# Kernel optimization log

Measured on AMD Instinct MI355X. Metric: run time of the kernel, lower is better.

The kernel has to match this reference:

```python
import jax, jax.numpy as jnp
import numpy as np

B, NWORD, HID = 4, 24, 512


def setup_inputs() -> dict:
    key = jax.random.key(0)
    ks = jax.random.split(key, 7)
    H = HID
    scale_in = 1.0 / np.sqrt(H)
    return {
        "seqt": jax.random.normal(ks[0], (B, NWORD, 2 * H), dtype=jnp.float32),
        # ins_input_linearity: Linear(H -> 5H) with bias
        "Wi": jax.random.normal(ks[1], (5 * H, H), dtype=jnp.float32) * scale_in,
        "bi": jnp.zeros((5 * H,), dtype=jnp.float32),
        # ins_state_linearity: Linear(H -> 5H) with bias (bias init: forget slots = 1)
        "Ws": jax.random.normal(ks[2], (5 * H, H), dtype=jnp.float32) * scale_in,
        "bs": jnp.zeros((5 * H,), dtype=jnp.float32).at[H:2 * H].set(1.0),
        # ins_bilinearity: BilinearSimilarity(2H, 2H) -> scalar x^T W y
        "Wbil": jax.random.normal(ks[3], (2 * H, 2 * H), dtype=jnp.float32) * (1.0 / (2.0 * H)),
    }


def reference(seqt, Wi, bi, Ws, bs, Wbil):
    """Inside pass (do_inside) of DioLstm in training mode (soft_sum over splits).

    Chart cell (left, L) covers words [left, left+L]. Returns root v = concat(h, c).
    """
    Bn, n, twoH = seqt.shape
    H = twoH // 2
    # ins_bias buffer: ones on the two forget-gate slots [H:3H]
    ins_bias = jnp.zeros((5 * H,), dtype=seqt.dtype).at[H:3 * H].set(1.0)

    def single(seq):  # seq: [n, 2H]
        chartH = jnp.zeros((n, n, H), seq.dtype).at[:, 0].set(seq[:, :H])
        chartC = jnp.zeros((n, n, H), seq.dtype).at[:, 0].set(seq[:, H:])
        chartS = jnp.zeros((n, n), seq.dtype)  # leaf scores are 0
        for L in range(1, n):  # span length - 1 (static unroll over diagonals)
            P = n - L  # number of spans on this diagonal
            lefts = jnp.arange(P)[:, None]          # [P,1]
            ksplit = jnp.arange(L)[None, :]          # [1,L]
            # left child: (left, k); right child: (left+k+1, L-1-k)
            lH = chartH[lefts, ksplit]; lC = chartC[lefts, ksplit]; lS = chartS[lefts, ksplit]
            ridx = lefts + ksplit + 1
            rlen = jnp.broadcast_to(L - 1 - ksplit, ridx.shape)
            rH = chartH[ridx, rlen]; rC = chartC[ridx, rlen]; rS = chartS[ridx, rlen]
            lv = jnp.concatenate([lH, lC], axis=-1)  # [P,L,2H]
            rv = jnp.concatenate([rH, rC], axis=-1)
            # bilinear compatibility + child scores
            compat = jnp.einsum('pki,ij,pkj->pk', lv, Wbil, rv) + lS + rS  # [P,L]
            # projected_input + projected_state (sum once; gate slices of the sum)
            proj = (lH @ Wi.T + bi + ins_bias) + (rH @ Ws.T + bs)  # [P,L,5H]
            ig, lf, rf, g, og = jnp.split(proj, 5, axis=-1)
            ig = jax.nn.sigmoid(ig); lf = jax.nn.sigmoid(lf); rf = jax.nn.sigmoid(rf)
            g = jnp.tanh(g); og = jax.nn.sigmoid(og)
            mem = lf * lC + rf * rC + ig * g
            h = og * jnp.tanh(mem)  # [P,L,H]
            # soft_sum: torch.tensor(s_set) detaches scores -> stop_gradient on weights
            sw = jax.lax.stop_gradient(compat)
            w = jax.nn.softmax(sw, axis=-1)  # [P,L]
            Hnew = jnp.einsum('pk,pkh->ph', w, h)
            Cnew = jnp.einsum('pk,pkh->ph', w, mem)
            Snew = jnp.sum(w * sw, axis=-1)
            pidx = jnp.arange(P)
            chartH = chartH.at[pidx, L].set(Hnew)
            chartC = chartC.at[pidx, L].set(Cnew)
            chartS = chartS.at[pidx, L].set(Snew)
        # root cell v = concat(h, c)
        return jnp.concatenate([chartH[0, n - 1], chartC[0, n - 1]], axis=0)

    return jax.vmap(single)(seqt)  # [B, 2H]
```

## Files before the change

kernel.cpp:

```cpp
#include <hip/hip_runtime.h>
#include <math.h>

#define NB 4
#define NW 24
#define H 512
#define H2 1024
#define H5 2560
#define NCELL 300
#define NEED_BYTES ((size_t)72<<20)

static float* g_buf = nullptr;
__attribute__((constructor)) static void dio_alloc_ws(){
  (void)hipMalloc((void**)&g_buf, NEED_BYTES);
}

typedef __attribute__((ext_vector_type(8))) short bf16x8;
typedef __attribute__((ext_vector_type(4))) float f32x4;
typedef unsigned short ushort_t;

__device__ __forceinline__ int coff(int l){ return l*NW - (l*(l-1))/2; }
__device__ __forceinline__ float sigm(float x){ return 1.f/(1.f+__expf(-x)); }
__device__ __forceinline__ float ftanh(float x){ return 1.f - 2.f/(__expf(2.f*x)+1.f); }

__device__ __forceinline__ ushort_t f2b(float x){
  unsigned int u = __float_as_uint(x);
  u += 0x7FFF + ((u>>16)&1);
  return (ushort_t)(u>>16);
}
__device__ __forceinline__ float b2f(ushort_t h){
  return __uint_as_float(((unsigned int)h)<<16);
}
__device__ __forceinline__ void split_store(ushort_t* __restrict__ ph,
                                            ushort_t* __restrict__ pl,
                                            size_t idx, float x){
  ushort_t h = f2b(x);
  ph[idx] = h;
  pl[idx] = f2b(x - b2f(h));
}

__device__ __forceinline__ float compat_dot(const float* __restrict__ cU,
                                            const float* __restrict__ cH,
                                            const float* __restrict__ cC,
                                            const float* __restrict__ cS,
                                            int lc, int rc, int lane){
  const float4* U4  = (const float4*)(cU + (size_t)lc*H2);
  const float4* Hr4 = (const float4*)(cH + (size_t)rc*H);
  const float4* Cr4 = (const float4*)(cC + (size_t)rc*H);
  float p = 0.f;
  #pragma unroll
  for (int it=0; it<2; it++){
    float4 u = U4[lane + 64*it], h = Hr4[lane + 64*it];
    p += u.x*h.x + u.y*h.y + u.z*h.z + u.w*h.w;
  }
  #pragma unroll
  for (int it=0; it<2; it++){
    float4 u = U4[128 + lane + 64*it], c = Cr4[lane + 64*it];
    p += u.x*c.x + u.y*c.y + u.z*c.z + u.w*c.w;
  }
  #pragma unroll
  for (int off=32; off>0; off>>=1) p += __shfl_down(p, off);
  return p + cS[lc] + cS[rc];
}

__global__ void k_init(const float* __restrict__ seqt,
                       const float* __restrict__ Wi, const float* __restrict__ Ws,
                       const float* __restrict__ Wbil,
                       ushort_t* __restrict__ WiBh, ushort_t* __restrict__ WiBl,
                       ushort_t* __restrict__ WsBh, ushort_t* __restrict__ WsBl,
                       ushort_t* __restrict__ WbilTh, ushort_t* __restrict__ WbilTl,
                       float* __restrict__ cH, float* __restrict__ cC, float* __restrict__ cS,
                       ushort_t* __restrict__ cHbh, ushort_t* __restrict__ cHbl,
                       ushort_t* __restrict__ cCbh, ushort_t* __restrict__ cCbl){
  const int blk = blockIdx.x, t = threadIdx.x;
  if (blk < 10240){
    int i = blk*256 + t;
    const int n = H5*H;
    if (i < n) split_store(WiBh, WiBl, i, Wi[i]);
    else       split_store(WsBh, WsBl, i-n, Ws[i-n]);
  } else if (blk < 11264){
    __shared__ float tile[32][33];
    int tb = blk - 10240;
    int tr = (tb>>5)*32, tc = (tb&31)*32;
    int tx = t & 31, ty = t >> 5;
    #pragma unroll
    for (int i=0;i<32;i+=8)
      tile[ty+i][tx] = Wbil[(size_t)(tr+ty+i)*H2 + tc+tx];
    __syncthreads();
    #pragma unroll
    for (int i=0;i<32;i+=8)
      split_store(WbilTh, WbilTl, (size_t)(tc+ty+i)*H2 + tr+tx, tile[tx][ty+i]);
  } else {
    int tid = (blk-11264)*256 + t;
    if (tid < NB*NW*H){
      int b = tid/(NW*H); int r = tid%(NW*H); int i = r/H; int d = r%H;
      size_t idx = (size_t)(b*NCELL + i)*H + d;
      float hv = seqt[(size_t)(b*NW+i)*H2 + d];
      float cv = seqt[(size_t)(b*NW+i)*H2 + H + d];
      cH[idx]=hv; cC[idx]=cv;
      split_store(cHbh,cHbl,idx,hv);
      split_store(cCbh,cCbl,idx,cv);
      if (d==0) cS[b*NCELL+i] = 0.f;
    }
  }
}

__device__ __forceinline__ void mfma3(f32x4& acc, bf16x8 ah, bf16x8 al,
                                      bf16x8 bh, bf16x8 bl){
  acc = __builtin_amdgcn_mfma_f32_16x16x32_bf16(ah, bh, acc, 0,0,0);
  acc = __builtin_amdgcn_mfma_f32_16x16x32_bf16(ah, bl, acc, 0,0,0);
  acc = __builtin_amdgcn_mfma_f32_16x16x32_bf16(al, bh, acc, 0,0,0);
}

__global__ void __launch_bounds__(512)
k_projN(const ushort_t* __restrict__ WiBh, const ushort_t* __restrict__ WiBl,
        const ushort_t* __restrict__ WsBh, const ushort_t* __restrict__ WsBl,
        const ushort_t* __restrict__ WbilTh, const ushort_t* __restrict__ WbilTl,
        const float* __restrict__ bi, const float* __restrict__ bs,
        const ushort_t* __restrict__ cHbh, const ushort_t* __restrict__ cHbl,
        const ushort_t* __restrict__ cCbh, const ushort_t* __restrict__ cCbl,
        float* __restrict__ cPI, float* __restrict__ cPS, float* __restrict__ cU,
        int d, int P)
{
  __shared__ f32x4 red[8][64];
  const int t = threadIdx.x, wave = t>>6, lane = t&63;
  const int jt = blockIdx.x;
  const int m0 = blockIdx.y*16;
  const int Mtot = NB*P;
  const int nm = min(16, Mtot-m0);

  int kind, j0;
  if (jt < 160){ kind=0; j0 = jt*16; }
  else if (jt < 320){ kind=1; j0 = (jt-160)*16; }
  else { kind=2; j0 = (jt-320)*16; }

  const int r = lane & 15;
  const int q = lane >> 4;

  int mg = m0 + (r < nm ? r : 0);
  const size_t arow = (size_t)((mg/P)*NCELL + coff(d) + mg%P)*H;

  f32x4 acc = {0.f,0.f,0.f,0.f};

  if (kind < 2){
    const ushort_t* bh_ = (kind==0 ? WiBh : WsBh) + (size_t)(j0+r)*H;
    const ushort_t* bl_ = (kind==0 ? WiBl : WsBl) + (size_t)(j0+r)*H;
    const int ks = wave*64 + q*8;
    bf16x8 fah[2], fal[2], fbh[2], fbl[2];
    #pragma unroll
    for (int s=0;s<2;s++){
      const int ko = ks + s*32;
      fah[s] = *(const bf16x8*)(cHbh + arow + ko);
      fal[s] = *(const bf16x8*)(cHbl + arow + ko);
      fbh[s] = *(const bf16x8*)(bh_ + ko);
      fbl[s] = *(const bf16x8*)(bl_ + ko);
    }
    #pragma unroll
    for (int s=0;s<2;s++) mfma3(acc, fah[s], fal[s], fbh[s], fbl[s]);
  } else {
    const ushort_t* bh_ = WbilTh + (size_t)(j0+r)*H2;
    const ushort_t* bl_ = WbilTl + (size_t)(j0+r)*H2;
    const ushort_t* ah_ = (wave<4 ? cHbh : cCbh) + arow;
    const ushort_t* al_ = (wave<4 ? cHbl : cCbl) + arow;
    const int kg0 = wave*128;
    const int ka0 = kg0 & 511;
    bf16x8 fah[4], fal[4], fbh[4], fbl[4];
    #pragma unroll
    for (int s=0;s<4;s++){
      const int so = s*32 + q*8;
      fah[s] = *(const bf16x8*)(ah_ + ka0 + so);
      fal[s] = *(const bf16x8*)(al_ + ka0 + so);
      fbh[s] = *(const bf16x8*)(bh_ + kg0 + so);
      fbl[s] = *(const bf16x8*)(bl_ + kg0 + so);
    }
    #pragma unroll
    for (int s=0;s<4;s++) mfma3(acc, fah[s], fal[s], fbh[s], fbl[s]);
  }

  red[wave][lane] = acc;
  __syncthreads();
  if (wave == 0){
    f32x4 s0=red[0][lane], s1=red[1][lane], s2=red[2][lane], s3=red[3][lane];
    f32x4 s4=red[4][lane], s5=red[5][lane], s6=red[6][lane], s7=red[7][lane];
    f32x4 tot = ((s0+s1)+(s2+s3)) + ((s4+s5)+(s6+s7));
    const int jo = j0 + r;
    float bias = 0.f;
    if (kind==0) bias = bi[jo] + ((jo>=H && jo<3*H)?1.f:0.f);
    else if (kind==1) bias = bs[jo];
    #pragma unroll
    for (int reg=0; reg<4; reg++){
      const int m = q*4 + reg;
      if (m < nm){
        const int mg2 = m0 + m;
        const size_t cell = (size_t)((mg2/P)*NCELL + coff(d) + mg2%P);
        const float v = tot[reg];
        if (kind==0)      cPI[cell*H5 + jo] = v + bias;
        else if (kind==1) cPS[cell*H5 + jo] = v + bias;
        else              cU [cell*H2 + jo] = v;
      }
    }
  }
}

__global__ void __launch_bounds__(256)
k_combine3(const float* __restrict__ cPI, const float* __restrict__ cPS,
           const float* __restrict__ cU,
           float* __restrict__ cH, float* __restrict__ cC, float* __restrict__ cS,
           ushort_t* __restrict__ cHbh, ushort_t* __restrict__ cHbl,
           ushort_t* __restrict__ cCbh, ushort_t* __restrict__ cCbl,
           const float* __restrict__ compatR, float* __restrict__ compatW,
           int L, int P){
  const int t = threadIdx.x;
  const int lane = t & 63;
  const int wave = t >> 6;
  const int nphase = NB*P*16;
  const int blk = blockIdx.x;

  if (blk >= nphase){
    const int P1 = P-1;
    const int nterm = L-1;
    int tid = (blk-nphase)*4 + wave;
    if (P1 > 0 && nterm > 0 && tid < NB*P1*nterm){
      int cell1 = tid / nterm;
      int k = 1 + tid % nterm;
      int b = cell1 / P1, left = cell1 % P1;
      int lc = b*NCELL + coff(k) + left;
      int rc = b*NCELL + coff(L-k) + left+k+1;
      float v = compat_dot(cU, cH, cC, cS, lc, rc, lane);
      if (lane==0) compatW[(b*NW + left)*NW + k] = v;
    }
    return;
  }

  const int cellid = blk >> 4;
  const int dg = blk & 15;
  const int b = cellid / P;
  const int left = cellid % P;
  __shared__ float compat_s[32];
  __shared__ float wts_s[32];
  __shared__ float S_s;
  __shared__ float partH[8][32];
  __shared__ float partC[8][32];

  if (wave == 0){
    int lc = b*NCELL + left;
    int rc = b*NCELL + coff(L-1) + left+1;
    float v = compat_dot(cU, cH, cC, cS, lc, rc, lane);
    if (lane==0) compat_s[0] = v;
  } else if (wave == 1 && L >= 2){
    int lc = b*NCELL + coff(L-1) + left;
    int rc = b*NCELL + left+L;
    float v = compat_dot(cU, cH, cC, cS, lc, rc, lane);
    if (lane==0) compat_s[L-1] = v;
  }
  if (t >= 1 && t <= L-2) compat_s[t] = compatR[(b*NW + left)*NW + t];
  __syncthreads();
  if (t==0){
    float mx = -1e30f;
    for (int k=0;k<L;k++) mx = fmaxf(mx, compat_s[k]);
    float den = 0.f;
    for (int k=0;k<L;k++){ float e = __expf(compat_s[k]-mx); wts_s[k]=e; den+=e; }
    float inv = 1.f/den, S = 0.f;
    for (int k=0;k<L;k++){ wts_s[k]*=inv; S += wts_s[k]*compat_s[k]; }
    S_s = S;
  }
  __syncthreads();
  const int dloc = t & 31;
  const int dim = dg*32 + dloc;
  const int kpar = t >> 5;
  float aH = 0.f, aC = 0.f;
  for (int k=kpar; k<L; k+=8){
    float wk = wts_s[k];
    int lc = b*NCELL + coff(k) + left;
    int rc = b*NCELL + coff(L-1-k) + left+k+1;
    const float* PI = cPI + (size_t)lc*H5;
    const float* PS = cPS + (size_t)rc*H5;
    float p0 = PI[dim]     + PS[dim];
    float p1 = PI[H+dim]   + PS[H+dim];
    float p2 = PI[2*H+dim] + PS[2*H+dim];
    float p3 = PI[3*H+dim] + PS[3*H+dim];
    float p4 = PI[4*H+dim] + PS[4*H+dim];
    float lcv = cC[(size_t)lc*H + dim];
    float rcv = cC[(size_t)rc*H + dim];
    float mem = sigm(p1)*lcv + sigm(p2)*rcv + sigm(p0)*ftanh(p3);
    float h = sigm(p4)*ftanh(mem);
    aH += wk*h; aC += wk*mem;
  }
  if (kpar > 0){ partH[kpar][dloc]=aH; partC[kpar][dloc]=aC; }
  __syncthreads();
  if (kpar == 0){
    #pragma unroll
    for (int q=1;q<8;q++){ aH += partH[q][dloc]; aC += partC[q][dloc]; }
    size_t nc = (size_t)(b*NCELL + coff(L) + left);
    cH[nc*H + dim] = aH;
    cC[nc*H + dim] = aC;
    split_store(cHbh,cHbl, nc*H + dim, aH);
    split_store(cCbh,cCbl, nc*H + dim, aC);
    if (t==0 && dg==0) cS[nc] = S_s;
  }
}

__global__ void k_out(const float* __restrict__ cH, const float* __restrict__ cC,
                      float* __restrict__ out){
  int tid = blockIdx.x*256+threadIdx.x;
  if (tid >= NB*H2) return;
  int b = tid>>10, d = tid&1023;
  int cell = b*NCELL + 299;
  out[tid] = (d<H) ? cH[(size_t)cell*H + d] : cC[(size_t)cell*H + (d-H)];
}

extern "C" void kernel_launch(void* const* d_in, const int* in_sizes, int n_in,
                              void* d_out, int out_size, void* d_ws, size_t ws_size,
                              hipStream_t stream){
  const float* seqt = (const float*)d_in[0];
  const float* Wi   = (const float*)d_in[1];
  const float* bi   = (const float*)d_in[2];
  const float* Ws   = (const float*)d_in[3];
  const float* bs   = (const float*)d_in[4];
  const float* Wbil = (const float*)d_in[5];
  float* out = (float*)d_out;

  float* p = (ws_size >= NEED_BYTES && g_buf == nullptr) ? (float*)d_ws : g_buf;
  float* cH  = p; p += (size_t)NB*NCELL*H;
  float* cC  = p; p += (size_t)NB*NCELL*H;
  float* cS  = p; p += (size_t)NB*NCELL;
  float* cPI = p; p += (size_t)NB*NCELL*H5;
  float* cPS = p; p += (size_t)NB*NCELL*H5;
  float* cU  = p; p += (size_t)NB*NCELL*H2;
  float* compatA = p; p += (size_t)NB*NW*NW;
  float* compatB = p; p += (size_t)NB*NW*NW;
  ushort_t* u = (ushort_t*)p;
  ushort_t* WiBh   = u; u += (size_t)H5*H;
  ushort_t* WiBl   = u; u += (size_t)H5*H;
  ushort_t* WsBh   = u; u += (size_t)H5*H;
  ushort_t* WsBl   = u; u += (size_t)H5*H;
  ushort_t* WbilTh = u; u += (size_t)H2*H2;
  ushort_t* WbilTl = u; u += (size_t)H2*H2;
  ushort_t* cHbh   = u; u += (size_t)NB*NCELL*H;
  ushort_t* cHbl   = u; u += (size_t)NB*NCELL*H;
  ushort_t* cCbh   = u; u += (size_t)NB*NCELL*H;
  ushort_t* cCbl   = u; u += (size_t)NB*NCELL*H;

  k_init<<<11456, 256, 0, stream>>>(seqt, Wi, Ws, Wbil,
      WiBh, WiBl, WsBh, WsBl, WbilTh, WbilTl,
      cH, cC, cS, cHbh, cHbl, cCbh, cCbl);

  k_projN<<<dim3(384, (NB*NW+15)/16), 512, 0, stream>>>(
      WiBh, WiBl, WsBh, WsBl, WbilTh, WbilTl, bi, bs,
      cHbh, cHbl, cCbh, cCbl, cPI, cPS, cU, 0, NW);
  for (int L=1; L<NW; L++){
    int P = NW - L;
    int P1 = P-1, nterm = L-1;
    int wblk = (P1>0 && nterm>0) ? (NB*P1*nterm + 3)/4 : 0;
    float* bufR = (L&1) ? compatA : compatB;
    float* bufW = (L&1) ? compatB : compatA;
    k_combine3<<<NB*P*16 + wblk, 256, 0, stream>>>(
        cPI, cPS, cU, cH, cC, cS, cHbh, cHbl, cCbh, cCbl,
        bufR, bufW, L, P);
    if (L < NW-1)
      k_projN<<<dim3(384, (NB*P+15)/16), 512, 0, stream>>>(
          WiBh, WiBl, WsBh, WsBl, WbilTh, WbilTl, bi, bs,
          cHbh, cHbl, cCbh, cCbl, cPI, cPS, cU, L, P);
  }
  k_out<<<16, 256, 0, stream>>>(cH, cC, out);
}
```

Before: 617.7 us.

## Fuse all diagonal passes into one persistent kernel with grid barriers and LDS-resident weights

Replaces the per-diagonal chain of init, projection, combine and output launches with one persistent kernel of 512 blocks that separates phases with an atomic-counter grid barrier. Each projection block now keeps its 16-row slice of Wi/Ws or the transposed Wbil as hi/lo bf16 in swizzled shared memory for the whole run, so the split weights are no longer re-read from global memory every diagonal. Projection blocks loop over M tiles per wave instead of reducing eight K-slices across waves. This removes roughly 45 launch gaps. In exchange, all 512 blocks must be co-resident or the spin barrier deadlocks, and only 384 blocks do projection work.

```diff
diff --git a/kernel.cpp b/kernel.cpp
--- a/kernel.cpp
+++ b/kernel.cpp
@@ -7,6 +7,7 @@
 #define H2 1024
 #define H5 2560
 #define NCELL 300
+#define GRID 512
 #define NEED_BYTES ((size_t)72<<20)
 
 static float* g_buf = nullptr;
@@ -62,48 +63,6 @@
   return p + cS[lc] + cS[rc];
 }
 
-__global__ void k_init(const float* __restrict__ seqt,
-                       const float* __restrict__ Wi, const float* __restrict__ Ws,
-                       const float* __restrict__ Wbil,
-                       ushort_t* __restrict__ WiBh, ushort_t* __restrict__ WiBl,
-                       ushort_t* __restrict__ WsBh, ushort_t* __restrict__ WsBl,
-                       ushort_t* __restrict__ WbilTh, ushort_t* __restrict__ WbilTl,
-                       float* __restrict__ cH, float* __restrict__ cC, float* __restrict__ cS,
-                       ushort_t* __restrict__ cHbh, ushort_t* __restrict__ cHbl,
-                       ushort_t* __restrict__ cCbh, ushort_t* __restrict__ cCbl){
-  const int blk = blockIdx.x, t = threadIdx.x;
-  if (blk < 10240){
-    int i = blk*256 + t;
-    const int n = H5*H;
-    if (i < n) split_store(WiBh, WiBl, i, Wi[i]);
-    else       split_store(WsBh, WsBl, i-n, Ws[i-n]);
-  } else if (blk < 11264){
-    __shared__ float tile[32][33];
-    int tb = blk - 10240;
-    int tr = (tb>>5)*32, tc = (tb&31)*32;
-    int tx = t & 31, ty = t >> 5;
-    #pragma unroll
-    for (int i=0;i<32;i+=8)
-      tile[ty+i][tx] = Wbil[(size_t)(tr+ty+i)*H2 + tc+tx];
-    __syncthreads();
-    #pragma unroll
-    for (int i=0;i<32;i+=8)
-      split_store(WbilTh, WbilTl, (size_t)(tc+ty+i)*H2 + tr+tx, tile[tx][ty+i]);
-  } else {
-    int tid = (blk-11264)*256 + t;
-    if (tid < NB*NW*H){
-      int b = tid/(NW*H); int r = tid%(NW*H); int i = r/H; int d = r%H;
-      size_t idx = (size_t)(b*NCELL + i)*H + d;
-      float hv = seqt[(size_t)(b*NW+i)*H2 + d];
-      float cv = seqt[(size_t)(b*NW+i)*H2 + H + d];
-      cH[idx]=hv; cC[idx]=cv;
-      split_store(cHbh,cHbl,idx,hv);
-      split_store(cCbh,cCbl,idx,cv);
-      if (d==0) cS[b*NCELL+i] = 0.f;
-    }
-  }
-}
-
 __device__ __forceinline__ void mfma3(f32x4& acc, bf16x8 ah, bf16x8 al,
                                       bf16x8 bh, bf16x8 bl){
   acc = __builtin_amdgcn_mfma_f32_16x16x32_bf16(ah, bh, acc, 0,0,0);
@@ -111,81 +70,131 @@
   acc = __builtin_amdgcn_mfma_f32_16x16x32_bf16(al, bh, acc, 0,0,0);
 }
 
-__global__ void __launch_bounds__(512)
-k_projN(const ushort_t* __restrict__ WiBh, const ushort_t* __restrict__ WiBl,
-        const ushort_t* __restrict__ WsBh, const ushort_t* __restrict__ WsBl,
-        const ushort_t* __restrict__ WbilTh, const ushort_t* __restrict__ WbilTl,
-        const float* __restrict__ bi, const float* __restrict__ bs,
-        const ushort_t* __restrict__ cHbh, const ushort_t* __restrict__ cHbl,
-        const ushort_t* __restrict__ cCbh, const ushort_t* __restrict__ cCbl,
-        float* __restrict__ cPI, float* __restrict__ cPS, float* __restrict__ cU,
-        int d, int P)
+__device__ __forceinline__ void gbar(unsigned* cnt, unsigned target){
+  __syncthreads();
+  if (threadIdx.x == 0){
+    __hip_atomic_fetch_add(cnt, 1u, __ATOMIC_ACQ_REL, __HIP_MEMORY_SCOPE_AGENT);
+    while (__hip_atomic_load(cnt, __ATOMIC_RELAXED, __HIP_MEMORY_SCOPE_AGENT) < target)
+      __builtin_amdgcn_s_sleep(2);
+    __builtin_amdgcn_fence(__ATOMIC_ACQUIRE, "agent");
+  }
+  __syncthreads();
+}
+
+__device__ __forceinline__ void init_phase(
+    const float* __restrict__ seqt,
+    const float* __restrict__ Wi, const float* __restrict__ Ws,
+    const float* __restrict__ Wbil,
+    float* __restrict__ cH, float* __restrict__ cC, float* __restrict__ cS,
+    ushort_t* __restrict__ cHbh, ushort_t* __restrict__ cHbl,
+    ushort_t* __restrict__ cCbh, ushort_t* __restrict__ cCbl,
+    ushort_t* wlds)
 {
-  __shared__ f32x4 red[8][64];
-  const int t = threadIdx.x, wave = t>>6, lane = t&63;
+  const int t = threadIdx.x;
+  const int tid0 = blockIdx.x*256 + t;
+  const int nthr = gridDim.x*256;
+  for (int tid = tid0; tid < NB*NW*H; tid += nthr){
+    const int b = tid/(NW*H); const int rr = tid%(NW*H);
+    const int i = rr/H; const int dd = rr%H;
+    const size_t idx = (size_t)(b*NCELL + i)*H + dd;
+    const float hv = seqt[(size_t)(b*NW+i)*H2 + dd];
+    const float cv = seqt[(size_t)(b*NW+i)*H2 + H + dd];
+    cH[idx]=hv; cC[idx]=cv;
+    split_store(cHbh,cHbl,idx,hv);
+    split_store(cCbh,cCbl,idx,cv);
+    if (dd==0) cS[b*NCELL+i] = 0.f;
+  }
   const int jt = blockIdx.x;
-  const int m0 = blockIdx.y*16;
-  const int Mtot = NB*P;
-  const int nm = min(16, Mtot-m0);
-
+  char* wb = (char*)wlds;
+  if (jt < 320){
+    const float* mat = (jt<160) ? Wi : Ws;
+    const int j0 = (jt%160)*16;
+    for (int e = t; e < 16*512; e += 256){
+      const int row = e >> 9, col = e & 511;
+      const float x = mat[(size_t)(j0+row)*H + col];
+      const ushort_t h = f2b(x);
+      const int off = ((row<<10) + (col<<1)) ^ ((row&7)<<4);
+      *(ushort_t*)(wb + off) = h;
+      *(ushort_t*)(wb + 16384 + off) = f2b(x - b2f(h));
+    }
+  } else if (jt < 384){
+    const int j0 = (jt-320)*16;
+    for (int e = t; e < 16*1024; e += 256){
+      const int col = e >> 4, row = e & 15;
+      const float x = Wbil[(size_t)col*H2 + j0 + row];
+      const ushort_t h = f2b(x);
+      const int off = ((row<<11) + (col<<1)) ^ ((row&7)<<4);
+      *(ushort_t*)(wb + off) = h;
+      *(ushort_t*)(wb + 32768 + off) = f2b(x - b2f(h));
+    }
+  }
+}
+
+__device__ __forceinline__ void proj_phase(
+    const float* __restrict__ bi, const float* __restrict__ bs,
+    const ushort_t* __restrict__ cHbh, const ushort_t* __restrict__ cHbl,
+    const ushort_t* __restrict__ cCbh, const ushort_t* __restrict__ cCbl,
+    float* __restrict__ cPI, float* __restrict__ cPS, float* __restrict__ cU,
+    const ushort_t* wlds, int d, int P)
+{
+  const int jt = blockIdx.x;
+  if (jt >= 384) return;
+  const int t = threadIdx.x, wv = t>>6, lane = t&63;
+  const int r = lane & 15, q = lane >> 4;
   int kind, j0;
   if (jt < 160){ kind=0; j0 = jt*16; }
   else if (jt < 320){ kind=1; j0 = (jt-160)*16; }
   else { kind=2; j0 = (jt-320)*16; }
-
-  const int r = lane & 15;
-  const int q = lane >> 4;
-
-  int mg = m0 + (r < nm ? r : 0);
-  const size_t arow = (size_t)((mg/P)*NCELL + coff(d) + mg%P)*H;
-
-  f32x4 acc = {0.f,0.f,0.f,0.f};
-
-  if (kind < 2){
-    const ushort_t* bh_ = (kind==0 ? WiBh : WsBh) + (size_t)(j0+r)*H;
-    const ushort_t* bl_ = (kind==0 ? WiBl : WsBl) + (size_t)(j0+r)*H;
-    const int ks = wave*64 + q*8;
-    bf16x8 fah[2], fal[2], fbh[2], fbl[2];
+  const int Mtot = NB*P, mt = (Mtot+15)>>4;
+  const int swz = (r&7)<<4;
+  const char* wb = (const char*)wlds;
+  const int jo = j0 + r;
+  float bias = 0.f;
+  if (kind==0) bias = bi[jo] + ((jo>=H && jo<3*H)?1.f:0.f);
+  else if (kind==1) bias = bs[jo];
+
+  const f32x4 z4 = {0.f,0.f,0.f,0.f};
+  for (int mtile = wv; mtile < mt; mtile += 4){
+    const int m0 = mtile*16;
+    const int nm = min(16, Mtot - m0);
+    const int mg = m0 + (r < nm ? r : 0);
+    const size_t arow = (size_t)((mg/P)*NCELL + coff(d) + mg%P)*H;
+    f32x4 acc[8];
     #pragma unroll
-    for (int s=0;s<2;s++){
-      const int ko = ks + s*32;
-      fah[s] = *(const bf16x8*)(cHbh + arow + ko);
-      fal[s] = *(const bf16x8*)(cHbl + arow + ko);
-      fbh[s] = *(const bf16x8*)(bh_ + ko);
-      fbl[s] = *(const bf16x8*)(bl_ + ko);
-    }
-    #pragma unroll
-    for (int s=0;s<2;s++) mfma3(acc, fah[s], fal[s], fbh[s], fbl[s]);
-  } else {
-    const ushort_t* bh_ = WbilTh + (size_t)(j0+r)*H2;
-    const ushort_t* bl_ = WbilTl + (size_t)(j0+r)*H2;
-    const ushort_t* ah_ = (wave<4 ? cHbh : cCbh) + arow;
-    const ushort_t* al_ = (wave<4 ? cHbl : cCbl) + arow;
-    const int kg0 = wave*128;
-    const int ka0 = kg0 & 511;
-    bf16x8 fah[4], fal[4], fbh[4], fbl[4];
-    #pragma unroll
-    for (int s=0;s<4;s++){
-      const int so = s*32 + q*8;
-      fah[s] = *(const bf16x8*)(ah_ + ka0 + so);
-      fal[s] = *(const bf16x8*)(al_ + ka0 + so);
-      fbh[s] = *(const bf16x8*)(bh_ + kg0 + so);
-      fbl[s] = *(const bf16x8*)(bl_ + kg0 + so);
-    }
-    #pragma unroll
-    for (int s=0;s<4;s++) mfma3(acc, fah[s], fal[s], fbh[s], fbl[s]);
-  }
-
-  red[wave][lane] = acc;
-  __syncthreads();
-  if (wave == 0){
-    f32x4 s0=red[0][lane], s1=red[1][lane], s2=red[2][lane], s3=red[3][lane];
-    f32x4 s4=red[4][lane], s5=red[5][lane], s6=red[6][lane], s7=red[7][lane];
-    f32x4 tot = ((s0+s1)+(s2+s3)) + ((s4+s5)+(s6+s7));
-    const int jo = j0 + r;
-    float bias = 0.f;
-    if (kind==0) bias = bi[jo] + ((jo>=H && jo<3*H)?1.f:0.f);
-    else if (kind==1) bias = bs[jo];
+    for (int w=0;w<8;w++) acc[w] = z4;
+    if (kind < 2){
+      #pragma unroll
+      for (int w=0; w<8; w++){
+        #pragma unroll
+        for (int s=0;s<2;s++){
+          const int ko = w*64 + q*8 + s*32;
+          bf16x8 ah = *(const bf16x8*)(cHbh + arow + ko);
+          bf16x8 al = *(const bf16x8*)(cHbl + arow + ko);
+          const int bo = ((r<<10) + (ko<<1)) ^ swz;
+          bf16x8 bh = *(const bf16x8*)(wb + bo);
+          bf16x8 bl = *(const bf16x8*)(wb + 16384 + bo);
+          mfma3(acc[w], ah, al, bh, bl);
+        }
+      }
+    } else {
+      #pragma unroll
+      for (int w=0; w<8; w++){
+        const ushort_t* ah_ = (w<4 ? cHbh : cCbh) + arow;
+        const ushort_t* al_ = (w<4 ? cHbl : cCbl) + arow;
+        const int kg0 = w*128, ka0 = kg0 & 511;
+        #pragma unroll
+        for (int s=0;s<4;s++){
+          const int so = s*32 + q*8;
+          bf16x8 ah = *(const bf16x8*)(ah_ + ka0 + so);
+          bf16x8 al = *(const bf16x8*)(al_ + ka0 + so);
+          const int bo = ((r<<11) + ((kg0+so)<<1)) ^ swz;
+          bf16x8 bh = *(const bf16x8*)(wb + bo);
+          bf16x8 bl = *(const bf16x8*)(wb + 32768 + bo);
+          mfma3(acc[w], ah, al, bh, bl);
+        }
+      }
+    }
+    f32x4 tot = ((acc[0]+acc[1])+(acc[2]+acc[3])) + ((acc[4]+acc[5])+(acc[6]+acc[7]));
     #pragma unroll
     for (int reg=0; reg<4; reg++){
       const int m = q*4 + reg;
@@ -201,111 +210,144 @@
   }
 }
 
-__global__ void __launch_bounds__(256)
-k_combine3(const float* __restrict__ cPI, const float* __restrict__ cPS,
+__device__ __forceinline__ void combine_phase(
+           const float* __restrict__ cPI, const float* __restrict__ cPS,
            const float* __restrict__ cU,
            float* __restrict__ cH, float* __restrict__ cC, float* __restrict__ cS,
            ushort_t* __restrict__ cHbh, ushort_t* __restrict__ cHbl,
            ushort_t* __restrict__ cCbh, ushort_t* __restrict__ cCbl,
            const float* __restrict__ compatR, float* __restrict__ compatW,
            int L, int P){
-  const int t = threadIdx.x;
-  const int lane = t & 63;
-  const int wave = t >> 6;
-  const int nphase = NB*P*16;
-  const int blk = blockIdx.x;
-
-  if (blk >= nphase){
-    const int P1 = P-1;
-    const int nterm = L-1;
-    int tid = (blk-nphase)*4 + wave;
-    if (P1 > 0 && nterm > 0 && tid < NB*P1*nterm){
-      int cell1 = tid / nterm;
-      int k = 1 + tid % nterm;
-      int b = cell1 / P1, left = cell1 % P1;
-      int lc = b*NCELL + coff(k) + left;
-      int rc = b*NCELL + coff(L-k) + left+k+1;
-      float v = compat_dot(cU, cH, cC, cS, lc, rc, lane);
-      if (lane==0) compatW[(b*NW + left)*NW + k] = v;
-    }
-    return;
-  }
-
-  const int cellid = blk >> 4;
-  const int dg = blk & 15;
-  const int b = cellid / P;
-  const int left = cellid % P;
   __shared__ float compat_s[32];
   __shared__ float wts_s[32];
   __shared__ float S_s;
   __shared__ float partH[8][32];
   __shared__ float partC[8][32];
-
-  if (wave == 0){
-    int lc = b*NCELL + left;
-    int rc = b*NCELL + coff(L-1) + left+1;
-    float v = compat_dot(cU, cH, cC, cS, lc, rc, lane);
-    if (lane==0) compat_s[0] = v;
-  } else if (wave == 1 && L >= 2){
-    int lc = b*NCELL + coff(L-1) + left;
-    int rc = b*NCELL + left+L;
-    float v = compat_dot(cU, cH, cC, cS, lc, rc, lane);
-    if (lane==0) compat_s[L-1] = v;
-  }
-  if (t >= 1 && t <= L-2) compat_s[t] = compatR[(b*NW + left)*NW + t];
-  __syncthreads();
-  if (t==0){
-    float mx = -1e30f;
-    for (int k=0;k<L;k++) mx = fmaxf(mx, compat_s[k]);
-    float den = 0.f;
-    for (int k=0;k<L;k++){ float e = __expf(compat_s[k]-mx); wts_s[k]=e; den+=e; }
-    float inv = 1.f/den, S = 0.f;
-    for (int k=0;k<L;k++){ wts_s[k]*=inv; S += wts_s[k]*compat_s[k]; }
-    S_s = S;
-  }
-  __syncthreads();
-  const int dloc = t & 31;
-  const int dim = dg*32 + dloc;
-  const int kpar = t >> 5;
-  float aH = 0.f, aC = 0.f;
-  for (int k=kpar; k<L; k+=8){
-    float wk = wts_s[k];
-    int lc = b*NCELL + coff(k) + left;
-    int rc = b*NCELL + coff(L-1-k) + left+k+1;
-    const float* PI = cPI + (size_t)lc*H5;
-    const float* PS = cPS + (size_t)rc*H5;
-    float p0 = PI[dim]     + PS[dim];
-    float p1 = PI[H+dim]   + PS[H+dim];
-    float p2 = PI[2*H+dim] + PS[2*H+dim];
-    float p3 = PI[3*H+dim] + PS[3*H+dim];
-    float p4 = PI[4*H+dim] + PS[4*H+dim];
-    float lcv = cC[(size_t)lc*H + dim];
-    float rcv = cC[(size_t)rc*H + dim];
-    float mem = sigm(p1)*lcv + sigm(p2)*rcv + sigm(p0)*ftanh(p3);
-    float h = sigm(p4)*ftanh(mem);
-    aH += wk*h; aC += wk*mem;
-  }
-  if (kpar > 0){ partH[kpar][dloc]=aH; partC[kpar][dloc]=aC; }
-  __syncthreads();
-  if (kpar == 0){
-    #pragma unroll
-    for (int q=1;q<8;q++){ aH += partH[q][dloc]; aC += partC[q][dloc]; }
-    size_t nc = (size_t)(b*NCELL + coff(L) + left);
-    cH[nc*H + dim] = aH;
-    cC[nc*H + dim] = aC;
-    split_store(cHbh,cHbl, nc*H + dim, aH);
-    split_store(cCbh,cCbl, nc*H + dim, aC);
-    if (t==0 && dg==0) cS[nc] = S_s;
-  }
-}
-
-__global__ void k_out(const float* __restrict__ cH, const float* __restrict__ cC,
-                      float* __restrict__ out){
-  int tid = blockIdx.x*256+threadIdx.x;
-  if (tid >= NB*H2) return;
-  int b = tid>>10, d = tid&1023;
-  int cell = b*NCELL + 299;
-  out[tid] = (d<H) ? cH[(size_t)cell*H + d] : cC[(size_t)cell*H + (d-H)];
+  const int t = threadIdx.x;
+  const int lane = t & 63;
+  const int wave = t >> 6;
+  const int nphase = NB*P*16;
+  const int P1 = P-1, nterm = L-1;
+  const int nwt = (P1>0 && nterm>0) ? NB*P1*nterm : 0;
+  const int wblk = (nwt+3)>>2;
+
+  for (int u = blockIdx.x; u < nphase + wblk; u += gridDim.x){
+    if (u >= nphase){
+      const int tid = (u-nphase)*4 + wave;
+      if (tid < nwt){
+        const int cell1 = tid / nterm;
+        const int k = 1 + tid % nterm;
+        const int b = cell1 / P1, left = cell1 % P1;
+        const int lc = b*NCELL + coff(k) + left;
+        const int rc = b*NCELL + coff(L-k) + left+k+1;
+        float v = compat_dot(cU, cH, cC, cS, lc, rc, lane);
+        if (lane==0) compatW[(b*NW + left)*NW + k] = v;
+      }
+      continue;
+    }
+    const int cellid = u >> 4;
+    const int dg = u & 15;
+    const int b = cellid / P;
+    const int left = cellid % P;
+    __syncthreads();
+    if (wave == 0){
+      const int lc = b*NCELL + left;
+      const int rc = b*NCELL + coff(L-1) + left+1;
+      float v = compat_dot(cU, cH, cC, cS, lc, rc, lane);
+      if (lane==0) compat_s[0] = v;
+    } else if (wave == 1 && L >= 2){
+      const int lc = b*NCELL + coff(L-1) + left;
+      const int rc = b*NCELL + left+L;
+      float v = compat_dot(cU, cH, cC, cS, lc, rc, lane);
+      if (lane==0) compat_s[L-1] = v;
+    }
+    if (t >= 1 && t <= L-2) compat_s[t] = compatR[(b*NW + left)*NW + t];
+    __syncthreads();
+    if (t==0){
+      float mx = -1e30f;
+      for (int k=0;k<L;k++) mx = fmaxf(mx, compat_s[k]);
+      float den = 0.f;
+      for (int k=0;k<L;k++){ float e = __expf(compat_s[k]-mx); wts_s[k]=e; den+=e; }
+      float inv = 1.f/den, S = 0.f;
+      for (int k=0;k<L;k++){ wts_s[k]*=inv; S += wts_s[k]*compat_s[k]; }
+      S_s = S;
+    }
+    __syncthreads();
+    const int dloc = t & 31;
+    const int dim = dg*32 + dloc;
+    const int kpar = t >> 5;
+    float aH = 0.f, aC = 0.f;
+    for (int k=kpar; k<L; k+=8){
+      float wk = wts_s[k];
+      const int lc = b*NCELL + coff(k) + left;
+      const int rc = b*NCELL + coff(L-1-k) + left+k+1;
+      const float* PI = cPI + (size_t)lc*H5;
+      const float* PS = cPS + (size_t)rc*H5;
+      float p0 = PI[dim]     + PS[dim];
+      float p1 = PI[H+dim]   + PS[H+dim];
+      float p2 = PI[2*H+dim] + PS[2*H+dim];
+      float p3 = PI[3*H+dim] + PS[3*H+dim];
+      float p4 = PI[4*H+dim] + PS[4*H+dim];
+      float lcv = cC[(size_t)lc*H + dim];
+      float rcv = cC[(size_t)rc*H + dim];
+      float mem = sigm(p1)*lcv + sigm(p2)*rcv + sigm(p0)*ftanh(p3);
+      float h = sigm(p4)*ftanh(mem);
+      aH += wk*h; aC += wk*mem;
+    }
+    if (kpar > 0){ partH[kpar][dloc]=aH; partC[kpar][dloc]=aC; }
+    __syncthreads();
+    if (kpar == 0){
+      #pragma unroll
+      for (int qq=1;qq<8;qq++){ aH += partH[qq][dloc]; aC += partC[qq][dloc]; }
+      const size_t nc = (size_t)(b*NCELL + coff(L) + left);
+      cH[nc*H + dim] = aH;
+      cC[nc*H + dim] = aC;
+      split_store(cHbh,cHbl, nc*H + dim, aH);
+      split_store(cCbh,cCbl, nc*H + dim, aC);
+      if (t==0 && dg==0) cS[nc] = S_s;
+    }
+  }
+}
+
+__global__ void __launch_bounds__(256, 2)
+k_persist(const float* __restrict__ seqt,
+          const float* __restrict__ Wi, const float* __restrict__ bi,
+          const float* __restrict__ Ws, const float* __restrict__ bs,
+          const float* __restrict__ Wbil,
+          float* __restrict__ cH, float* __restrict__ cC, float* __restrict__ cS,
+          float* __restrict__ cPI, float* __restrict__ cPS, float* __restrict__ cU,
+          float* __restrict__ compatA, float* __restrict__ compatB,
+          ushort_t* __restrict__ cHbh, ushort_t* __restrict__ cHbl,
+          ushort_t* __restrict__ cCbh, ushort_t* __restrict__ cCbl,
+          float* __restrict__ out, unsigned* __restrict__ barcnt)
+{
+  __shared__ __attribute__((aligned(16))) ushort_t wlds[32768];
+  unsigned gen = 0;
+
+  init_phase(seqt, Wi, Ws, Wbil, cH, cC, cS, cHbh, cHbl, cCbh, cCbl, wlds);
+  gbar(barcnt, (++gen)*gridDim.x);
+
+  proj_phase(bi, bs, cHbh, cHbl, cCbh, cCbl, cPI, cPS, cU, wlds, 0, NW);
+  gbar(barcnt, (++gen)*gridDim.x);
+
+  for (int L=1; L<NW; L++){
+    const int P = NW - L;
+    const float* bufR = (L&1) ? compatA : compatB;
+    float* bufW = (L&1) ? compatB : compatA;
+    combine_phase(cPI, cPS, cU, cH, cC, cS, cHbh, cHbl, cCbh, cCbl,
+                  bufR, bufW, L, P);
+    gbar(barcnt, (++gen)*gridDim.x);
+    if (L < NW-1){
+      proj_phase(bi, bs, cHbh, cHbl, cCbh, cCbl, cPI, cPS, cU, wlds, L, P);
+      gbar(barcnt, (++gen)*gridDim.x);
+    }
+  }
+  const int tid = blockIdx.x*256 + threadIdx.x;
+  if (tid < NB*H2){
+    const int b = tid>>10, dd = tid&1023;
+    const int cell = b*NCELL + 299;
+    out[tid] = (dd<H) ? cH[(size_t)cell*H + dd] : cC[(size_t)cell*H + (dd-H)];
+  }
 }
 
 extern "C" void kernel_launch(void* const* d_in, const int* in_sizes, int n_in,
@@ -329,37 +371,14 @@
   float* compatA = p; p += (size_t)NB*NW*NW;
   float* compatB = p; p += (size_t)NB*NW*NW;
   ushort_t* u = (ushort_t*)p;
-  ushort_t* WiBh   = u; u += (size_t)H5*H;
-  ushort_t* WiBl   = u; u += (size_t)H5*H;
-  ushort_t* WsBh   = u; u += (size_t)H5*H;
-  ushort_t* WsBl   = u; u += (size_t)H5*H;
-  ushort_t* WbilTh = u; u += (size_t)H2*H2;
-  ushort_t* WbilTl = u; u += (size_t)H2*H2;
-  ushort_t* cHbh   = u; u += (size_t)NB*NCELL*H;
-  ushort_t* cHbl   = u; u += (size_t)NB*NCELL*H;
-  ushort_t* cCbh   = u; u += (size_t)NB*NCELL*H;
-  ushort_t* cCbl   = u; u += (size_t)NB*NCELL*H;
-
-  k_init<<<11456, 256, 0, stream>>>(seqt, Wi, Ws, Wbil,
-      WiBh, WiBl, WsBh, WsBl, WbilTh, WbilTl,
-      cH, cC, cS, cHbh, cHbl, cCbh, cCbl);
-
-  k_projN<<<dim3(384, (NB*NW+15)/16), 512, 0, stream>>>(
-      WiBh, WiBl, WsBh, WsBl, WbilTh, WbilTl, bi, bs,
-      cHbh, cHbl, cCbh, cCbl, cPI, cPS, cU, 0, NW);
-  for (int L=1; L<NW; L++){
-    int P = NW - L;
-    int P1 = P-1, nterm = L-1;
-    int wblk = (P1>0 && nterm>0) ? (NB*P1*nterm + 3)/4 : 0;
-    float* bufR = (L&1) ? compatA : compatB;
-    float* bufW = (L&1) ? compatB : compatA;
-    k_combine3<<<NB*P*16 + wblk, 256, 0, stream>>>(
-        cPI, cPS, cU, cH, cC, cS, cHbh, cHbl, cCbh, cCbl,
-        bufR, bufW, L, P);
-    if (L < NW-1)
-      k_projN<<<dim3(384, (NB*P+15)/16), 512, 0, stream>>>(
-          WiBh, WiBl, WsBh, WsBl, WbilTh, WbilTl, bi, bs,
-          cHbh, cHbl, cCbh, cCbl, cPI, cPS, cU, L, P);
-  }
-  k_out<<<16, 256, 0, stream>>>(cH, cC, out);
-}
+  ushort_t* cHbh = u; u += (size_t)NB*NCELL*H;
+  ushort_t* cHbl = u; u += (size_t)NB*NCELL*H;
+  ushort_t* cCbh = u; u += (size_t)NB*NCELL*H;
+  ushort_t* cCbl = u; u += (size_t)NB*NCELL*H;
+  unsigned* barcnt = (unsigned*)u;
+
+  (void)hipMemsetAsync(barcnt, 0, 64, stream);
+  k_persist<<<GRID, 256, 0, stream>>>(seqt, Wi, bi, Ws, bs, Wbil,
+      cH, cC, cS, cPI, cPS, cU, compatA, compatB,
+      cHbh, cHbl, cCbh, cCbl, out, barcnt);
+}
```

After: 2.432 ms. 294% more time.

## Stage weight tiles in LDS and loop over M tiles within each block

Applied to the files above, without the earlier changes.

The projection kernel now launches one block per 16-column weight tile instead of a 2D grid over weight and row tiles. Each block loads its hi/lo bf16 weight slice once into swizzled shared memory and loops over all row tiles, with waves split into K halves and reduced through shared memory. This avoids re-reading the same weights from global memory for every M tile. In exchange it uses up to 64KB of LDS, which lowers occupancy, serialises the M tiles inside a block, and adds two barriers per round.

```diff
diff --git a/kernel.cpp b/kernel.cpp
--- a/kernel.cpp
+++ b/kernel.cpp
@@ -112,7 +112,7 @@
 }
 
 __global__ void __launch_bounds__(512)
-k_projN(const ushort_t* __restrict__ WiBh, const ushort_t* __restrict__ WiBl,
+k_proj2(const ushort_t* __restrict__ WiBh, const ushort_t* __restrict__ WiBl,
         const ushort_t* __restrict__ WsBh, const ushort_t* __restrict__ WsBl,
         const ushort_t* __restrict__ WbilTh, const ushort_t* __restrict__ WbilTl,
         const float* __restrict__ bi, const float* __restrict__ bs,
@@ -121,83 +121,124 @@
         float* __restrict__ cPI, float* __restrict__ cPS, float* __restrict__ cU,
         int d, int P)
 {
+  __shared__ __attribute__((aligned(16))) ushort_t wlds[32768];
   __shared__ f32x4 red[8][64];
-  const int t = threadIdx.x, wave = t>>6, lane = t&63;
+  const int t = threadIdx.x, wv = t>>6, lane = t&63;
+  const int r = lane & 15;
+  const int q = lane >> 4;
   const int jt = blockIdx.x;
-  const int m0 = blockIdx.y*16;
-  const int Mtot = NB*P;
-  const int nm = min(16, Mtot-m0);
 
   int kind, j0;
   if (jt < 160){ kind=0; j0 = jt*16; }
   else if (jt < 320){ kind=1; j0 = (jt-160)*16; }
   else { kind=2; j0 = (jt-320)*16; }
 
-  const int r = lane & 15;
-  const int q = lane >> 4;
-
-  int mg = m0 + (r < nm ? r : 0);
-  const size_t arow = (size_t)((mg/P)*NCELL + coff(d) + mg%P)*H;
-
-  f32x4 acc = {0.f,0.f,0.f,0.f};
-
+  char* wb = (char*)wlds;
   if (kind < 2){
-    const ushort_t* bh_ = (kind==0 ? WiBh : WsBh) + (size_t)(j0+r)*H;
-    const ushort_t* bl_ = (kind==0 ? WiBl : WsBl) + (size_t)(j0+r)*H;
-    const int ks = wave*64 + q*8;
-    bf16x8 fah[2], fal[2], fbh[2], fbl[2];
+    const ushort_t* srcH = (kind==0 ? WiBh : WsBh) + (size_t)j0*H;
+    const ushort_t* srcL = (kind==0 ? WiBl : WsBl) + (size_t)j0*H;
     #pragma unroll
-    for (int s=0;s<2;s++){
-      const int ko = ks + s*32;
-      fah[s] = *(const bf16x8*)(cHbh + arow + ko);
-      fal[s] = *(const bf16x8*)(cHbl + arow + ko);
-      fbh[s] = *(const bf16x8*)(bh_ + ko);
-      fbl[s] = *(const bf16x8*)(bl_ + ko);
-    }
+    for (int e = t; e < 1024; e += 512){
+      const int row = e >> 6, c0 = (e & 63) << 3;
+      bf16x8 vh = *(const bf16x8*)(srcH + (size_t)row*H + c0);
+      bf16x8 vl = *(const bf16x8*)(srcL + (size_t)row*H + c0);
+      const int off = ((row<<10) + (c0<<1)) ^ ((row&7)<<4);
+      *(bf16x8*)(wb + off) = vh;
+      *(bf16x8*)(wb + 16384 + off) = vl;
+    }
+  } else {
+    const ushort_t* srcH = WbilTh + (size_t)j0*H2;
+    const ushort_t* srcL = WbilTl + (size_t)j0*H2;
     #pragma unroll
-    for (int s=0;s<2;s++) mfma3(acc, fah[s], fal[s], fbh[s], fbl[s]);
-  } else {
-    const ushort_t* bh_ = WbilTh + (size_t)(j0+r)*H2;
-    const ushort_t* bl_ = WbilTl + (size_t)(j0+r)*H2;
-    const ushort_t* ah_ = (wave<4 ? cHbh : cCbh) + arow;
-    const ushort_t* al_ = (wave<4 ? cHbl : cCbl) + arow;
-    const int kg0 = wave*128;
-    const int ka0 = kg0 & 511;
-    bf16x8 fah[4], fal[4], fbh[4], fbl[4];
-    #pragma unroll
-    for (int s=0;s<4;s++){
-      const int so = s*32 + q*8;
-      fah[s] = *(const bf16x8*)(ah_ + ka0 + so);
-      fal[s] = *(const bf16x8*)(al_ + ka0 + so);
-      fbh[s] = *(const bf16x8*)(bh_ + kg0 + so);
-      fbl[s] = *(const bf16x8*)(bl_ + kg0 + so);
-    }
-    #pragma unroll
-    for (int s=0;s<4;s++) mfma3(acc, fah[s], fal[s], fbh[s], fbl[s]);
-  }
-
-  red[wave][lane] = acc;
+    for (int e = t; e < 2048; e += 512){
+      const int row = e >> 7, c0 = (e & 127) << 3;
+      bf16x8 vh = *(const bf16x8*)(srcH + (size_t)row*H2 + c0);
+      bf16x8 vl = *(const bf16x8*)(srcL + (size_t)row*H2 + c0);
+      const int off = ((row<<11) + (c0<<1)) ^ ((row&7)<<4);
+      *(bf16x8*)(wb + off) = vh;
+      *(bf16x8*)(wb + 32768 + off) = vl;
+    }
+  }
   __syncthreads();
-  if (wave == 0){
-    f32x4 s0=red[0][lane], s1=red[1][lane], s2=red[2][lane], s3=red[3][lane];
-    f32x4 s4=red[4][lane], s5=red[5][lane], s6=red[6][lane], s7=red[7][lane];
-    f32x4 tot = ((s0+s1)+(s2+s3)) + ((s4+s5)+(s6+s7));
-    const int jo = j0 + r;
-    float bias = 0.f;
-    if (kind==0) bias = bi[jo] + ((jo>=H && jo<3*H)?1.f:0.f);
-    else if (kind==1) bias = bs[jo];
-    #pragma unroll
-    for (int reg=0; reg<4; reg++){
-      const int m = q*4 + reg;
-      if (m < nm){
-        const int mg2 = m0 + m;
-        const size_t cell = (size_t)((mg2/P)*NCELL + coff(d) + mg2%P);
-        const float v = tot[reg];
-        if (kind==0)      cPI[cell*H5 + jo] = v + bias;
-        else if (kind==1) cPS[cell*H5 + jo] = v + bias;
-        else              cU [cell*H2 + jo] = v;
+
+  const int Mtot = NB*P, mt = (Mtot+15)>>4;
+  const int swz = (r&7)<<4;
+  const int jo = j0 + r;
+  float bias = 0.f;
+  if (kind==0) bias = bi[jo] + ((jo>=H && jo<3*H)?1.f:0.f);
+  else if (kind==1) bias = bs[jo];
+
+  const f32x4 z4 = {0.f,0.f,0.f,0.f};
+  const int units = 2*mt;
+  const int rounds = (units + 7) >> 3;
+  for (int rd = 0; rd < rounds; rd++){
+    const int u = rd*8 + wv;
+    const int half = u & 1;
+    const int mtile = u >> 1;
+    f32x4 sA = z4;
+    int m0 = 0, nm = 0;
+    if (u < units){
+      m0 = mtile*16;
+      nm = min(16, Mtot - m0);
+      const int mg = m0 + (r < nm ? r : 0);
+      const size_t arow = (size_t)((mg/P)*NCELL + coff(d) + mg%P)*H;
+      f32x4 acc[4];
+      #pragma unroll
+      for (int wi=0;wi<4;wi++) acc[wi] = z4;
+      if (kind < 2){
+        #pragma unroll
+        for (int wi=0; wi<4; wi++){
+          const int w = half*4 + wi;
+          #pragma unroll
+          for (int s=0;s<2;s++){
+            const int ko = w*64 + q*8 + s*32;
+            bf16x8 ah = *(const bf16x8*)(cHbh + arow + ko);
+            bf16x8 al = *(const bf16x8*)(cHbl + arow + ko);
+            const int bo = ((r<<10) + (ko<<1)) ^ swz;
+            bf16x8 bh = *(const bf16x8*)(wb + bo);
+            bf16x8 bl = *(const bf16x8*)(wb + 16384 + bo);
+            mfma3(acc[wi], ah, al, bh, bl);
+          }
+        }
+      } else {
+        const ushort_t* ah_ = (half==0 ? cHbh : cCbh) + arow;
+        const ushort_t* al_ = (half==0 ? cHbl : cCbl) + arow;
+        #pragma unroll
+        for (int wi=0; wi<4; wi++){
+          const int w = half*4 + wi;
+          const int kg0 = w*128, ka0 = kg0 & 511;
+          #pragma unroll
+          for (int s=0;s<4;s++){
+            const int so = s*32 + q*8;
+            bf16x8 ah = *(const bf16x8*)(ah_ + ka0 + so);
+            bf16x8 al = *(const bf16x8*)(al_ + ka0 + so);
+            const int bo = ((r<<11) + ((kg0+so)<<1)) ^ swz;
+            bf16x8 bh = *(const bf16x8*)(wb + bo);
+            bf16x8 bl = *(const bf16x8*)(wb + 32768 + bo);
+            mfma3(acc[wi], ah, al, bh, bl);
+          }
+        }
       }
-    }
+      sA = (acc[0]+acc[1]) + (acc[2]+acc[3]);
+    }
+    red[wv][lane] = sA;
+    __syncthreads();
+    if (half==0 && u < units){
+      f32x4 tot = red[wv][lane] + red[wv|1][lane];
+      #pragma unroll
+      for (int reg=0; reg<4; reg++){
+        const int m = q*4 + reg;
+        if (m < nm){
+          const int mg2 = m0 + m;
+          const size_t cell = (size_t)((mg2/P)*NCELL + coff(d) + mg2%P);
+          const float v = tot[reg];
+          if (kind==0)      cPI[cell*H5 + jo] = v + bias;
+          else if (kind==1) cPS[cell*H5 + jo] = v + bias;
+          else              cU [cell*H2 + jo] = v;
+        }
+      }
+    }
+    __syncthreads();
   }
 }
 
@@ -344,7 +385,7 @@
       WiBh, WiBl, WsBh, WsBl, WbilTh, WbilTl,
       cH, cC, cS, cHbh, cHbl, cCbh, cCbl);
 
-  k_projN<<<dim3(384, (NB*NW+15)/16), 512, 0, stream>>>(
+  k_proj2<<<384, 512, 0, stream>>>(
       WiBh, WiBl, WsBh, WsBl, WbilTh, WbilTl, bi, bs,
       cHbh, cHbl, cCbh, cCbl, cPI, cPS, cU, 0, NW);
   for (int L=1; L<NW; L++){
@@ -357,7 +398,7 @@
         cPI, cPS, cU, cH, cC, cS, cHbh, cHbl, cCbh, cCbl,
         bufR, bufW, L, P);
     if (L < NW-1)
-      k_projN<<<dim3(384, (NB*P+15)/16), 512, 0, stream>>>(
+      k_proj2<<<384, 512, 0, stream>>>(
           WiBh, WiBl, WsBh, WsBl, WbilTh, WbilTl, bi, bs,
           cHbh, cHbl, cCbh, cCbl, cPI, cPS, cU, L, P);
   }
```

Measured after the change: 584.1 us. 5.4% less time.
